# Optimization experiments

Measured on AMD Instinct MI355X. Metric: run time of the kernel, lower is better.

Reference implementation:

```python
import jax, jax.numpy as jnp
import numpy as np

B, N, F, K, FILT = 256, 256, 128, 4, 256  # batch mols, max_atom, Fin, Chebyshev order, nb_filter
EPS = float(np.spacing(np.float32(0)))    # matches np.spacing(0) in original degree normalization
D2_FLOOR = 1e-12                          # numerical floor for sqrt of pairwise sq-dist


def setup_inputs() -> dict:
    key = jax.random.key(0)
    ks = jax.random.split(key, 6)
    x = jax.random.normal(ks[0], (B, N, F), dtype=jnp.float32)
    lap_in = 0.1 * jax.random.normal(ks[1], (B, N, N), dtype=jnp.float32)  # input per-mol Laplacian
    n_atoms = jax.random.randint(ks[2], (B,), 64, N + 1, dtype=jnp.int32)  # ragged mol sizes
    r1 = float(np.sqrt(6.0 / (F + F)))
    M_L = jax.random.uniform(ks[3], (F, F), jnp.float32, -r1, r1)          # Mahalanobis metric
    r2 = float(np.sqrt(6.0 / (F * K + FILT)))
    weight = jax.random.uniform(ks[4], (F * K, FILT), jnp.float32, -r2, r2)
    bias = jnp.zeros((FILT,), jnp.float32)
    return {"x": x, "lap_in": lap_in, "n_atoms": n_atoms, "M_L": M_L, "weight": weight, "bias": bias}


def reference(x, lap_in, n_atoms, M_L, weight, bias):
    # mask[b,n] = 1 for real atoms, 0 for padding (replaces per-mol tf.slice + pad)
    mask = (jnp.arange(N)[None, :] < n_atoms[:, None]).astype(x.dtype)       # [B,N]
    x = x * mask[..., None]

    # ---- learned Laplacian: Mahalanobis RBF affinity + sym degree normalization ----
    xw = jnp.einsum('bnf,fg->bng', x, M_L)                                   # x @ M_L
    sq = jnp.sum(xw * xw, axis=-1)                                           # [B,N]
    d2 = sq[:, :, None] + sq[:, None, :] - 2.0 * jnp.einsum('bif,bjf->bij', xw, xw)
    eye = jnp.eye(N, dtype=x.dtype)
    off = mask[:, :, None] * mask[:, None, :] * (1.0 - eye)                  # valid off-diag pairs
    d2_safe = jnp.where(off > 0, jnp.maximum(d2, D2_FLOOR), 1.0)
    W = jnp.exp(-jnp.sqrt(d2_safe)) * off                                    # W[i,j]=exp(-dist), diag 0
    deg = jnp.sum(W, axis=1) + EPS                                           # W symmetric: axis0==axis1
    dinv = jnp.where(mask > 0, 1.0 / jnp.sqrt(deg), 0.0)                     # D^{-1/2} (0 on padding)
    # L = I - D^{-1/2} W D^{-1/2} (intended math of the original py_func)
    L_learn = eye[None] * mask[:, :, None] - dinv[:, :, None] * W * dinv[:, None, :]
    L = L_learn + lap_in * (mask[:, :, None] * mask[:, None, :])             # L + sliced input LL

    # ---- Chebyshev recurrence: x0=x, x1=Lx, xk = 2 L x_{k-1} - x_{k-2} ----
    x0 = x
    x1 = jnp.einsum('bij,bjf->bif', L, x0)
    xs = [x0, x1]
    for _ in range(2, K):
        x2 = 2.0 * jnp.einsum('bij,bjf->bif', L, x1) - x0
        xs.append(x2)
        x0, x1 = x1, x2
    # stack -> [B,N,F,K] then flatten (f,k) row-major, matching reshape([K,M,F])->transpose([1,2,0])->reshape([M,K*F])
    xc = jnp.stack(xs, axis=-1).reshape(B, N, F * K)

    out = jnp.einsum('bnd,do->bno', xc, weight) + bias                       # [B,N,FILT]
    out = jax.nn.relu(out * mask[..., None])                                 # pad-to-max_atom + relu
    return out, L_learn
```

## Files before the change

kernel.cpp:

```cpp
#include <hip/hip_runtime.h>
#include <math.h>

typedef __bf16 bf16;
typedef __bf16 bf16x8 __attribute__((ext_vector_type(8)));
typedef __bf16 bf16x4 __attribute__((ext_vector_type(4)));
typedef float f32x4 __attribute__((ext_vector_type(4)));

constexpr int cB = 256, cN = 256, cF = 128, cO = 256;
constexpr int BN = cB * cN;
constexpr float D2_FLOOR = 1e-12f;
constexpr float EPS_F = 1.401298464324817e-45f;

constexpr size_t OFF_XC  = 0;
constexpr size_t OFF_XW  = OFF_XC + (size_t)BN * 512 * 2;
constexpr size_t OFF_X0T = OFF_XW + (size_t)BN * 128 * 2;
constexpr size_t OFF_LB  = OFF_X0T + (size_t)cB * cF * cN * 2;
constexpr size_t OFF_WB  = OFF_LB + (size_t)cB * cN * cN * 2;
constexpr size_t OFF_WT  = OFF_WB + (size_t)cB * cN * cN * 2;
constexpr size_t OFF_MT  = OFF_WT + 512 * 256 * 2;
constexpr size_t OFF_SQ  = OFF_MT + 128 * 128 * 2;
constexpr size_t OFF_DEG = OFF_SQ + (size_t)BN * 4;

__device__ __forceinline__ bf16x8 gfrag(const bf16* __restrict__ p, int ld,
                                        int lane, int k0) {
  return *(const bf16x8*)(p + (size_t)(lane & 15) * ld + k0 + 8 * (lane >> 4));
}

__device__ __forceinline__ f32x4 mfma(bf16x8 a, bf16x8 b, f32x4 c) {
  return __builtin_amdgcn_mfma_f32_16x16x32_bf16(a, b, c, 0, 0, 0);
}

__device__ __forceinline__ void gll16(const void* g, void* l) {
  __builtin_amdgcn_global_load_lds((const __attribute__((address_space(1))) void*)g,
                                   (__attribute__((address_space(3))) void*)l, 16, 0, 0);
}

__global__ __launch_bounds__(256) void k_prep(const float* __restrict__ x,
                                              const int* __restrict__ na_p,
                                              bf16* __restrict__ xc,
                                              bf16* __restrict__ x0T) {
  __shared__ __align__(16) bf16 T[64][132];
  int b = blockIdx.x >> 2, i0 = (blockIdx.x & 3) * 64;
  int tid = threadIdx.x;
  int na = na_p[b];
#pragma unroll
  for (int it = 0; it < 8; ++it) {
    int ir = it * 8 + (tid >> 5);
    int f0 = (tid & 31) * 4;
    int i = i0 + ir;
    float m = (i < na) ? 1.f : 0.f;
    float4 v = *(const float4*)(x + ((size_t)b * cN + i) * cF + f0);
    bf16x4 pk = {(bf16)(v.x * m), (bf16)(v.y * m), (bf16)(v.z * m), (bf16)(v.w * m)};
    *(bf16x4*)(xc + ((size_t)b * cN + i) * 512 + f0) = pk;
    *(bf16x4*)(&T[ir][f0]) = pk;
  }
  __syncthreads();
  int f = tid >> 1, half = tid & 1;
  bf16* od = x0T + ((size_t)b * cF + f) * cN + i0 + half * 32;
#pragma unroll
  for (int c = 0; c < 32; c += 4) {
    int ii = half * 32 + c;
    bf16x4 pk = {T[ii][f], T[ii + 1][f], T[ii + 2][f], T[ii + 3][f]};
    *(bf16x4*)(od + c) = pk;
  }
}

__global__ __launch_bounds__(256) void k_wt(const float* __restrict__ wgt,
                                            const float* __restrict__ ML,
                                            bf16* __restrict__ Wt,
                                            bf16* __restrict__ MT) {
  int id = blockIdx.x * 256 + threadIdx.x;
  if (id < 512 * 256) {
    int o = id >> 9, d = id & 511;
    int k = d >> 7, f = d & 127;
    Wt[id] = (bf16)wgt[(f * 4 + k) * 256 + o];
  } else {
    int id2 = id - 512 * 256;
    if (id2 < 128 * 128) {
      int g = id2 >> 7, f = id2 & 127;
      MT[id2] = (bf16)ML[f * 128 + g];
    }
  }
}

__global__ __launch_bounds__(256, 2) void k_xw2(const bf16* __restrict__ xc,
                                                const bf16* __restrict__ MT,
                                                bf16* __restrict__ xw,
                                                float* __restrict__ sq) {
  __shared__ float sqb[128];
  int tid = threadIdx.x, wid = tid >> 6, lane = tid & 63;
  int r0 = blockIdx.x * 128;
  const bf16* A = xc + (size_t)r0 * 512;
  const bf16* Bg = MT + (size_t)(wid * 32) * 128;
  f32x4 acc[8][2] = {};
#pragma unroll
  for (int ks = 0; ks < 4; ++ks) {
    int k0 = ks * 32;
    bf16x8 b0 = gfrag(Bg, 128, lane, k0);
    bf16x8 b1 = gfrag(Bg + 16 * 128, 128, lane, k0);
#pragma unroll
    for (int mf = 0; mf < 8; ++mf) {
      bf16x8 a = gfrag(A + (size_t)mf * 16 * 512, 512, lane, k0);
      acc[mf][0] = mfma(a, b0, acc[mf][0]);
      acc[mf][1] = mfma(a, b1, acc[mf][1]);
    }
  }
  if (tid < 128) sqb[tid] = 0.f;
  __syncthreads();
  int hi = lane >> 4, il = lane & 15;
#pragma unroll
  for (int mf = 0; mf < 8; ++mf) {
#pragma unroll
    for (int r = 0; r < 4; ++r) {
      int row = r0 + mf * 16 + 4 * hi + r;
      float s = 0.f;
#pragma unroll
      for (int nf = 0; nf < 2; ++nf) {
        bf16 v = (bf16)acc[mf][nf][r];
        xw[(size_t)row * cF + wid * 32 + nf * 16 + il] = v;
        float f = (float)v;
        s = fmaf(f, f, s);
      }
      s += __shfl_xor(s, 1); s += __shfl_xor(s, 2);
      s += __shfl_xor(s, 4); s += __shfl_xor(s, 8);
      if (il == 0) atomicAdd(&sqb[mf * 16 + 4 * hi + r], s);
    }
  }
  __syncthreads();
  if (tid < 128) sq[r0 + tid] = sqb[tid];
}

__global__ __launch_bounds__(512, 2) void k_gram2(const bf16* __restrict__ xw,
                                                  const float* __restrict__ sq,
                                                  const int* __restrict__ na_p,
                                                  bf16* __restrict__ Wb16,
                                                  float* __restrict__ deg) {
  __shared__ float lsq[256];
  __shared__ float degl[128];
  int bx = blockIdx.x;
  int b = bx >> 1, i0 = (bx & 1) * 128;
  int tid = threadIdx.x, wid = tid >> 6, lane = tid & 63;
  int wm = wid >> 2, wn = wid & 3;
  if (tid < 256) lsq[tid] = sq[b * cN + tid];
  if (tid < 128) degl[tid] = 0.f;
  const bf16* X = xw + (size_t)b * cN * cF;
  const bf16* Ag = X + (size_t)(i0 + wm * 64) * cF;
  const bf16* Bg = X + (size_t)(wn * 64) * cF;
  f32x4 acc[4][4] = {};
#pragma unroll
  for (int ks = 0; ks < 4; ++ks) {
    int k0 = ks * 32;
    bf16x8 bb[4];
#pragma unroll
    for (int nf = 0; nf < 4; ++nf) bb[nf] = gfrag(Bg + (size_t)nf * 16 * cF, cF, lane, k0);
#pragma unroll
    for (int mf = 0; mf < 4; ++mf) {
      bf16x8 a = gfrag(Ag + (size_t)mf * 16 * cF, cF, lane, k0);
#pragma unroll
      for (int nf = 0; nf < 4; ++nf) acc[mf][nf] = mfma(a, bb[nf], acc[mf][nf]);
    }
  }
  __syncthreads();
  int na = na_p[b];
  int hi = lane >> 4, il = lane & 15;
#pragma unroll
  for (int mf = 0; mf < 4; ++mf) {
#pragma unroll
    for (int r = 0; r < 4; ++r) {
      int i = i0 + wm * 64 + mf * 16 + 4 * hi + r;
      float sqi = lsq[i];
      bool mi = i < na;
      float rs = 0.f;
#pragma unroll
      for (int nf = 0; nf < 4; ++nf) {
        int j = wn * 64 + nf * 16 + il;
        float w = 0.f;
        if (mi && j < na && i != j) {
          float d2 = fmaxf(sqi + lsq[j] - 2.f * acc[mf][nf][r], D2_FLOOR);
          w = __expf(-sqrtf(d2));
        }
        Wb16[((size_t)b * cN + i) * cN + j] = (bf16)w;
        rs += w;
      }
      rs += __shfl_xor(rs, 1); rs += __shfl_xor(rs, 2);
      rs += __shfl_xor(rs, 4); rs += __shfl_xor(rs, 8);
      if (il == 0) atomicAdd(&degl[i - i0], rs);
    }
  }
  __syncthreads();
  if (tid < 128) deg[b * cN + i0 + tid] = degl[tid];
}

__global__ __launch_bounds__(256) void k_Lassm(const bf16* __restrict__ Wb16,
                                               const float* __restrict__ deg,
                                               const float* __restrict__ lap,
                                               const int* __restrict__ na_p,
                                               bf16* __restrict__ Lb,
                                               float* __restrict__ llearn) {
  int tid = threadIdx.x;
  size_t e = ((size_t)blockIdx.x * 256 + tid) * 4;
  int b = (int)(e >> 16);
  int na = na_p[b];
  __shared__ float dinvl[256];
  if (tid < 256) dinvl[tid] = (tid < na) ? 1.f / sqrtf(deg[b * cN + tid] + EPS_F) : 0.f;
  __syncthreads();
  int j = (int)(e & 255);
  int i = (int)((e >> 8) & 255);
  bf16x4 w4 = *(const bf16x4*)(Wb16 + e);
  float4 lp = *(const float4*)(lap + e);
  float di = dinvl[i];
  float mi = (i < na) ? 1.f : 0.f;
  float4 ll;
  bf16x4 lo;
#pragma unroll
  for (int c = 0; c < 4; ++c) {
    int jj = j + c;
    float v = -di * (float)w4[c] * dinvl[jj];
    if (i == jj && i < na) v += 1.f;
    (&ll.x)[c] = v;
    float mj = (jj < na) ? 1.f : 0.f;
    lo[c] = (bf16)(v + (&lp.x)[c] * mi * mj);
  }
  *(float4*)(llearn + e) = ll;
  *(bf16x4*)(Lb + e) = lo;
}

__device__ __forceinline__ void cheb_step(const bf16* __restrict__ Lm,
                                          const char* Bsrc, const char* Ppp,
                                          char* Odst, bf16* __restrict__ xcm,
                                          int kcol, int wid, int lane, bool haspp,
                                          bool wlds) {
  int hi = lane >> 4, il = lane & 15;
  int i0w = wid * 32;
  f32x4 acc[2][8] = {};
#pragma unroll
  for (int ks = 0; ks < 8; ++ks) {
    int k0 = ks * 32;
    bf16x8 a0 = gfrag(Lm + (size_t)i0w * cN, cN, lane, k0);
    bf16x8 a1 = gfrag(Lm + (size_t)(i0w + 16) * cN, cN, lane, k0);
#pragma unroll
    for (int nf = 0; nf < 8; ++nf) {
      int f = nf * 16 + il;
      const char* p = Bsrc + f * 512 + ((64 * ks + 16 * hi) ^ ((il & 7) << 4));
      bf16x8 bb = *(const bf16x8*)p;
      acc[0][nf] = mfma(a0, bb, acc[0][nf]);
      acc[1][nf] = mfma(a1, bb, acc[1][nf]);
    }
  }
#pragma unroll
  for (int mf = 0; mf < 2; ++mf) {
    int ib = i0w + mf * 16 + 4 * hi;
#pragma unroll
    for (int nf = 0; nf < 8; ++nf) {
      int f = nf * 16 + il;
      int cb = (2 * ib) ^ ((il & 7) << 4);
      bf16x4 o;
      if (haspp) {
        bf16x4 pp = *(const bf16x4*)(Ppp + f * 512 + cb);
#pragma unroll
        for (int r = 0; r < 4; ++r) o[r] = (bf16)(2.f * acc[mf][nf][r] - (float)pp[r]);
      } else {
#pragma unroll
        for (int r = 0; r < 4; ++r) o[r] = (bf16)acc[mf][nf][r];
      }
      if (wlds) *(bf16x4*)(Odst + f * 512 + cb) = o;
#pragma unroll
      for (int r = 0; r < 4; ++r)
        xcm[(size_t)(ib + r) * 512 + kcol + f] = o[r];
    }
  }
}

__global__ __launch_bounds__(512, 1) void k_cheb_f(const bf16* __restrict__ x0T,
                                                   const bf16* __restrict__ Lb,
                                                   bf16* __restrict__ xc) {
  __shared__ __align__(16) char XB[2][65536];
  int b = blockIdx.x;
  int tid = threadIdx.x, wid = tid >> 6, lane = tid & 63;
  const bf16* Lm = Lb + (size_t)b * cN * cN;
  bf16* xcm = xc + (size_t)b * cN * 512;
  const char* src = (const char*)(x0T + (size_t)b * cF * cN);
#pragma unroll
  for (int it = 0; it < 8; ++it) {
    int beta = it * 8192 + tid * 16;
    int f = beta >> 9, c = beta & 511;
    gll16(src + f * 512 + (c ^ ((f & 7) << 4)), XB[0] + beta);
  }
  __syncthreads();
  cheb_step(Lm, XB[0], nullptr, XB[1], xcm, 128, wid, lane, false, true);
  __syncthreads();
  cheb_step(Lm, XB[1], XB[0], XB[0], xcm, 256, wid, lane, true, true);
  __syncthreads();
  cheb_step(Lm, XB[0], XB[1], nullptr, xcm, 384, wid, lane, true, false);
}

__global__ __launch_bounds__(256, 2) void k_out2(const bf16* __restrict__ xc,
                                                 const bf16* __restrict__ Wt,
                                                 const float* __restrict__ bias,
                                                 const int* __restrict__ na_p,
                                                 float* __restrict__ out) {
  int tid = threadIdx.x, wid = tid >> 6, lane = tid & 63;
  int r0 = blockIdx.x * 128;
  const bf16* A = xc + (size_t)r0 * 512;
  const bf16* Bg = Wt + (size_t)(wid * 64) * 512;
  f32x4 acc[8][4] = {};
#pragma unroll 4
  for (int ks = 0; ks < 16; ++ks) {
    int k0 = ks * 32;
    bf16x8 bb[4];
#pragma unroll
    for (int nf = 0; nf < 4; ++nf) bb[nf] = gfrag(Bg + (size_t)nf * 16 * 512, 512, lane, k0);
#pragma unroll
    for (int mf = 0; mf < 8; ++mf) {
      bf16x8 a = gfrag(A + (size_t)mf * 16 * 512, 512, lane, k0);
#pragma unroll
      for (int nf = 0; nf < 4; ++nf) acc[mf][nf] = mfma(a, bb[nf], acc[mf][nf]);
    }
  }
  int na = na_p[r0 >> 8];
  int hi = lane >> 4, il = lane & 15;
#pragma unroll
  for (int nf = 0; nf < 4; ++nf) {
    int o = wid * 64 + nf * 16 + il;
    float bo = bias[o];
#pragma unroll
    for (int mf = 0; mf < 8; ++mf) {
#pragma unroll
      for (int r = 0; r < 4; ++r) {
        int row = r0 + mf * 16 + 4 * hi + r;
        float m = ((row & 255) < na) ? 1.f : 0.f;
        out[(size_t)row * cO + o] = fmaxf((acc[mf][nf][r] + bo) * m, 0.f);
      }
    }
  }
}

extern "C" void kernel_launch(void* const* d_in, const int* in_sizes, int n_in,
                              void* d_out, int out_size, void* d_ws, size_t ws_size,
                              hipStream_t stream) {
  const float* x    = (const float*)d_in[0];
  const float* lap  = (const float*)d_in[1];
  const int*   na   = (const int*)d_in[2];
  const float* M_L  = (const float*)d_in[3];
  const float* wgt  = (const float*)d_in[4];
  const float* bias = (const float*)d_in[5];

  float* out    = (float*)d_out;
  float* llearn = out + (size_t)BN * cO;

  char* ws = (char*)d_ws;
  bf16*  xc  = (bf16*)(ws + OFF_XC);
  bf16*  xw  = (bf16*)(ws + OFF_XW);
  bf16*  x0T = (bf16*)(ws + OFF_X0T);
  bf16*  Lb  = (bf16*)(ws + OFF_LB);
  bf16*  Wb  = (bf16*)(ws + OFF_WB);
  bf16*  Wt  = (bf16*)(ws + OFF_WT);
  bf16*  MT  = (bf16*)(ws + OFF_MT);
  float* sqb = (float*)(ws + OFF_SQ);
  float* deg = (float*)(ws + OFF_DEG);

  k_prep<<<dim3(1024), 256, 0, stream>>>(x, na, xc, x0T);
  k_wt<<<dim3(576), 256, 0, stream>>>(wgt, M_L, Wt, MT);
  k_xw2<<<dim3(512), 256, 0, stream>>>(xc, MT, xw, sqb);
  k_gram2<<<dim3(512), 512, 0, stream>>>(xw, sqb, na, Wb, deg);
  k_Lassm<<<dim3(16384), 256, 0, stream>>>(Wb, deg, lap, na, Lb, llearn);
  k_cheb_f<<<dim3(cB), 512, 0, stream>>>(x0T, Lb, xc);
  k_out2<<<dim3(512), 256, 0, stream>>>(xc, Wt, bias, na, out);
}
```

Measured before the change: 380.6 us.

## Shrink row tiles, split gram over j, widen Lassm vectors, raise occupancy

k_xw2 and k_out2 now process 64 rows per block instead of 128, with launch bounds raised to 4 blocks per CU, so twice as many blocks run with fewer accumulators each. k_gram2 splits each molecule into four 128x128 tiles handled by 256-thread blocks and accumulates degree with global atomics into a buffer zeroed by a memset. k_Lassm handles 8 elements per thread with wider loads and stores. The aim is better occupancy and load balance across CUs, at the cost of more global atomics, less operand reuse per block and an extra memset launch.

```diff
diff --git a/kernel.cpp b/kernel.cpp
--- a/kernel.cpp
+++ b/kernel.cpp
@@ -83,33 +83,33 @@
   }
 }
 
-__global__ __launch_bounds__(256, 2) void k_xw2(const bf16* __restrict__ xc,
+__global__ __launch_bounds__(256, 4) void k_xw2(const bf16* __restrict__ xc,
                                                 const bf16* __restrict__ MT,
                                                 bf16* __restrict__ xw,
                                                 float* __restrict__ sq) {
-  __shared__ float sqb[128];
+  __shared__ float sqb[64];
   int tid = threadIdx.x, wid = tid >> 6, lane = tid & 63;
-  int r0 = blockIdx.x * 128;
+  int r0 = blockIdx.x * 64;
   const bf16* A = xc + (size_t)r0 * 512;
   const bf16* Bg = MT + (size_t)(wid * 32) * 128;
-  f32x4 acc[8][2] = {};
+  f32x4 acc[4][2] = {};
 #pragma unroll
   for (int ks = 0; ks < 4; ++ks) {
     int k0 = ks * 32;
     bf16x8 b0 = gfrag(Bg, 128, lane, k0);
     bf16x8 b1 = gfrag(Bg + 16 * 128, 128, lane, k0);
 #pragma unroll
-    for (int mf = 0; mf < 8; ++mf) {
+    for (int mf = 0; mf < 4; ++mf) {
       bf16x8 a = gfrag(A + (size_t)mf * 16 * 512, 512, lane, k0);
       acc[mf][0] = mfma(a, b0, acc[mf][0]);
       acc[mf][1] = mfma(a, b1, acc[mf][1]);
     }
   }
-  if (tid < 128) sqb[tid] = 0.f;
+  if (tid < 64) sqb[tid] = 0.f;
   __syncthreads();
   int hi = lane >> 4, il = lane & 15;
 #pragma unroll
-  for (int mf = 0; mf < 8; ++mf) {
+  for (int mf = 0; mf < 4; ++mf) {
 #pragma unroll
     for (int r = 0; r < 4; ++r) {
       int row = r0 + mf * 16 + 4 * hi + r;
@@ -127,25 +127,23 @@
     }
   }
   __syncthreads();
-  if (tid < 128) sq[r0 + tid] = sqb[tid];
-}
-
-__global__ __launch_bounds__(512, 2) void k_gram2(const bf16* __restrict__ xw,
+  if (tid < 64) sq[r0 + tid] = sqb[tid];
+}
+
+__global__ __launch_bounds__(256, 4) void k_gram2(const bf16* __restrict__ xw,
                                                   const float* __restrict__ sq,
                                                   const int* __restrict__ na_p,
                                                   bf16* __restrict__ Wb16,
                                                   float* __restrict__ deg) {
   __shared__ float lsq[256];
-  __shared__ float degl[128];
   int bx = blockIdx.x;
-  int b = bx >> 1, i0 = (bx & 1) * 128;
+  int b = bx >> 2, i0 = ((bx >> 1) & 1) * 128, j0 = (bx & 1) * 128;
   int tid = threadIdx.x, wid = tid >> 6, lane = tid & 63;
-  int wm = wid >> 2, wn = wid & 3;
-  if (tid < 256) lsq[tid] = sq[b * cN + tid];
-  if (tid < 128) degl[tid] = 0.f;
+  int wm = wid >> 1, wn = wid & 1;
+  lsq[tid] = sq[b * cN + tid];
   const bf16* X = xw + (size_t)b * cN * cF;
   const bf16* Ag = X + (size_t)(i0 + wm * 64) * cF;
-  const bf16* Bg = X + (size_t)(wn * 64) * cF;
+  const bf16* Bg = X + (size_t)(j0 + wn * 64) * cF;
   f32x4 acc[4][4] = {};
 #pragma unroll
   for (int ks = 0; ks < 4; ++ks) {
@@ -173,7 +171,7 @@
       float rs = 0.f;
 #pragma unroll
       for (int nf = 0; nf < 4; ++nf) {
-        int j = wn * 64 + nf * 16 + il;
+        int j = j0 + wn * 64 + nf * 16 + il;
         float w = 0.f;
         if (mi && j < na && i != j) {
           float d2 = fmaxf(sqi + lsq[j] - 2.f * acc[mf][nf][r], D2_FLOOR);
@@ -184,11 +182,9 @@
       }
       rs += __shfl_xor(rs, 1); rs += __shfl_xor(rs, 2);
       rs += __shfl_xor(rs, 4); rs += __shfl_xor(rs, 8);
-      if (il == 0) atomicAdd(&degl[i - i0], rs);
-    }
-  }
-  __syncthreads();
-  if (tid < 128) deg[b * cN + i0 + tid] = degl[tid];
+      if (il == 0) atomicAdd(&deg[b * cN + i], rs);
+    }
+  }
 }
 
 __global__ __launch_bounds__(256) void k_Lassm(const bf16* __restrict__ Wb16,
@@ -198,31 +194,34 @@
                                                bf16* __restrict__ Lb,
                                                float* __restrict__ llearn) {
   int tid = threadIdx.x;
-  size_t e = ((size_t)blockIdx.x * 256 + tid) * 4;
+  size_t e = ((size_t)blockIdx.x * 256 + tid) * 8;
   int b = (int)(e >> 16);
   int na = na_p[b];
   __shared__ float dinvl[256];
-  if (tid < 256) dinvl[tid] = (tid < na) ? 1.f / sqrtf(deg[b * cN + tid] + EPS_F) : 0.f;
+  dinvl[tid] = (tid < na) ? 1.f / sqrtf(deg[b * cN + tid] + EPS_F) : 0.f;
   __syncthreads();
   int j = (int)(e & 255);
   int i = (int)((e >> 8) & 255);
-  bf16x4 w4 = *(const bf16x4*)(Wb16 + e);
-  float4 lp = *(const float4*)(lap + e);
+  bf16x8 w8 = *(const bf16x8*)(Wb16 + e);
+  float4 lp0 = *(const float4*)(lap + e);
+  float4 lp1 = *(const float4*)(lap + e + 4);
   float di = dinvl[i];
   float mi = (i < na) ? 1.f : 0.f;
-  float4 ll;
-  bf16x4 lo;
-#pragma unroll
-  for (int c = 0; c < 4; ++c) {
+  float4 ll0, ll1;
+  bf16x8 lo;
+#pragma unroll
+  for (int c = 0; c < 8; ++c) {
     int jj = j + c;
-    float v = -di * (float)w4[c] * dinvl[jj];
+    float v = -di * (float)w8[c] * dinvl[jj];
     if (i == jj && i < na) v += 1.f;
-    (&ll.x)[c] = v;
+    float lpv = (c < 4) ? (&lp0.x)[c] : (&lp1.x)[c - 4];
+    if (c < 4) (&ll0.x)[c] = v; else (&ll1.x)[c - 4] = v;
     float mj = (jj < na) ? 1.f : 0.f;
-    lo[c] = (bf16)(v + (&lp.x)[c] * mi * mj);
-  }
-  *(float4*)(llearn + e) = ll;
-  *(bf16x4*)(Lb + e) = lo;
+    lo[c] = (bf16)(v + lpv * mi * mj);
+  }
+  *(float4*)(llearn + e) = ll0;
+  *(float4*)(llearn + e + 4) = ll1;
+  *(bf16x8*)(Lb + e) = lo;
 }
 
 __device__ __forceinline__ void cheb_step(const bf16* __restrict__ Lm,
@@ -294,16 +293,16 @@
   cheb_step(Lm, XB[0], XB[1], nullptr, xcm, 384, wid, lane, true, false);
 }
 
-__global__ __launch_bounds__(256, 2) void k_out2(const bf16* __restrict__ xc,
+__global__ __launch_bounds__(256, 4) void k_out2(const bf16* __restrict__ xc,
                                                  const bf16* __restrict__ Wt,
                                                  const float* __restrict__ bias,
                                                  const int* __restrict__ na_p,
                                                  float* __restrict__ out) {
   int tid = threadIdx.x, wid = tid >> 6, lane = tid & 63;
-  int r0 = blockIdx.x * 128;
+  int r0 = blockIdx.x * 64;
   const bf16* A = xc + (size_t)r0 * 512;
   const bf16* Bg = Wt + (size_t)(wid * 64) * 512;
-  f32x4 acc[8][4] = {};
+  f32x4 acc[4][4] = {};
 #pragma unroll 4
   for (int ks = 0; ks < 16; ++ks) {
     int k0 = ks * 32;
@@ -311,7 +310,7 @@
 #pragma unroll
     for (int nf = 0; nf < 4; ++nf) bb[nf] = gfrag(Bg + (size_t)nf * 16 * 512, 512, lane, k0);
 #pragma unroll
-    for (int mf = 0; mf < 8; ++mf) {
+    for (int mf = 0; mf < 4; ++mf) {
       bf16x8 a = gfrag(A + (size_t)mf * 16 * 512, 512, lane, k0);
 #pragma unroll
       for (int nf = 0; nf < 4; ++nf) acc[mf][nf] = mfma(a, bb[nf], acc[mf][nf]);
@@ -324,7 +323,7 @@
     int o = wid * 64 + nf * 16 + il;
     float bo = bias[o];
 #pragma unroll
-    for (int mf = 0; mf < 8; ++mf) {
+    for (int mf = 0; mf < 4; ++mf) {
 #pragma unroll
       for (int r = 0; r < 4; ++r) {
         int row = r0 + mf * 16 + 4 * hi + r;
@@ -359,11 +358,12 @@
   float* sqb = (float*)(ws + OFF_SQ);
   float* deg = (float*)(ws + OFF_DEG);
 
+  hipMemsetAsync(deg, 0, (size_t)BN * 4, stream);
   k_prep<<<dim3(1024), 256, 0, stream>>>(x, na, xc, x0T);
   k_wt<<<dim3(576), 256, 0, stream>>>(wgt, M_L, Wt, MT);
-  k_xw2<<<dim3(512), 256, 0, stream>>>(xc, MT, xw, sqb);
-  k_gram2<<<dim3(512), 512, 0, stream>>>(xw, sqb, na, Wb, deg);
-  k_Lassm<<<dim3(16384), 256, 0, stream>>>(Wb, deg, lap, na, Lb, llearn);
+  k_xw2<<<dim3(1024), 256, 0, stream>>>(xc, MT, xw, sqb);
+  k_gram2<<<dim3(1024), 256, 0, stream>>>(xw, sqb, na, Wb, deg);
+  k_Lassm<<<dim3(8192), 256, 0, stream>>>(Wb, deg, lap, na, Lb, llearn);
   k_cheb_f<<<dim3(cB), 512, 0, stream>>>(x0T, Lb, xc);
-  k_out2<<<dim3(512), 256, 0, stream>>>(xc, Wt, bias, na, out);
-}
+  k_out2<<<dim3(1024), 256, 0, stream>>>(xc, Wt, bias, na, out);
+}
```

Result: slower. 391.1 us (+2.8%).
